# Performance work log

Measured on AMD Instinct MI355X. Metric: run time of the kernel, lower is better.

The kernel has to match this reference:

```python
import jax, jax.numpy as jnp
import numpy as np

B, D_IN, D_OUT, N_CTRL = 8192, 512, 512, 8

def setup_inputs() -> dict:
    key = jax.random.key(0)
    k1, k2, k3, k4 = jax.random.split(key, 4)
    inputs = jax.random.normal(k1, (B, D_IN), dtype=jnp.float32)
    # routing weights: positive soft blend coefficients, normalized per sample
    raw = jax.random.uniform(k2, (B, N_CTRL), dtype=jnp.float32)
    weights = raw / jnp.sum(raw, axis=-1, keepdims=True)
    w = jax.random.normal(k3, (N_CTRL, D_IN, D_OUT), dtype=jnp.float32) * 0.05
    b = jax.random.normal(k4, (N_CTRL, D_OUT), dtype=jnp.float32) * 0.05
    return {"inputs": inputs, "weights": weights, "w": w, "b": b}

def reference(inputs, weights, w, b):
    # Original math: w_p = einsum('ji,imk->jmk', weights, w)  [B, D_IN, D_OUT]
    #                out = squeeze(inputs[:, None, :] @ w_p) + weights @ b
    # Fused equivalent avoiding the [B, D_IN, D_OUT] intermediate:
    # run all n_control expert matmuls, then blend by routing weights.
    per_expert = jnp.einsum('bi,cio->cbo', inputs, w)       # [C, B, D_OUT]
    out = jnp.einsum('bc,cbo->bo', weights, per_expert)     # [B, D_OUT]
    out = out + weights @ b                                 # blended bias [B, D_OUT]
    return out
```

## Files before the change

### kernel.cpp

```cpp
#include <hip/hip_runtime.h>

#define B_   8192
#define DIN  512
#define DOUT 512
#define NC   8
#define NCD  (NC * DIN)
#define KSPL 4

typedef float  f32x4 __attribute__((ext_vector_type(4)));
typedef short  s16x8 __attribute__((ext_vector_type(8)));
typedef unsigned short u16x4 __attribute__((ext_vector_type(4)));
typedef unsigned int   u32x4 __attribute__((ext_vector_type(4)));

__device__ __forceinline__ unsigned short f2bf(float f) {
  unsigned u = __builtin_bit_cast(unsigned, f);
  u += 0x7fffu + ((u >> 16) & 1u);
  return (unsigned short)(u >> 16);
}
__device__ __forceinline__ float bf2f(unsigned short h) {
  unsigned u = ((unsigned)h) << 16;
  return __builtin_bit_cast(float, u);
}
__device__ __forceinline__ unsigned cvtpk(float lo, float hi) {
  unsigned r;
  asm("v_cvt_pk_bf16_f32 %0, %1, %2" : "=v"(r) : "v"(lo), "v"(hi));
  return r;
}

__global__ void pack_xw_k(const f32x4* __restrict__ x, u16x4* __restrict__ xb,
                          const float* __restrict__ w, unsigned short* __restrict__ WtF) {
  __shared__ float tile[64][65];
  const int tid = threadIdx.x;
  if (blockIdx.x < 4096) {
    int gid = blockIdx.x * 256 + tid;
    f32x4 v = x[gid];
    u16x4 o;
    o[0] = f2bf(v[0]); o[1] = f2bf(v[1]); o[2] = f2bf(v[2]); o[3] = f2bf(v[3]);
    xb[gid] = o;
    return;
  }
  const int idx = blockIdx.x - 4096;
  const int kb = idx & 63, nb = idx >> 6;
  const int e = kb >> 3, ktl = kb & 7;
#pragma unroll
  for (int it = 0; it < 16; ++it) {
    int u = it * 256 + tid;
    int r = u >> 6, cc = u & 63;
    tile[r][cc] = w[(size_t)(e * 512 + ktl * 64 + r) * DOUT + nb * 64 + cc];
  }
  __syncthreads();
#pragma unroll
  for (int it = 0; it < 2; ++it) {
    int c = it * 256 + tid;
    int n16l = c >> 7, kk = (c >> 6) & 1, l = c & 63;
    int l15 = l & 15, lhi = l >> 4;
    int col_in = n16l * 16 + l15;
    int k_in   = kk * 32 + lhi * 8;
    int n16    = nb * 4 + n16l;
    u16x4 o0, o1;
    o0[0] = f2bf(tile[k_in + 0][col_in]); o0[1] = f2bf(tile[k_in + 1][col_in]);
    o0[2] = f2bf(tile[k_in + 2][col_in]); o0[3] = f2bf(tile[k_in + 3][col_in]);
    o1[0] = f2bf(tile[k_in + 4][col_in]); o1[1] = f2bf(tile[k_in + 5][col_in]);
    o1[2] = f2bf(tile[k_in + 6][col_in]); o1[3] = f2bf(tile[k_in + 7][col_in]);
    size_t base = ((((size_t)e * 32 + n16) * 8 + ktl) * 2 + kk) * 512 + l * 8;
    *(u16x4*)(WtF + base)     = o0;
    *(u16x4*)(WtF + base + 4) = o1;
  }
}

__global__ __launch_bounds__(256) void gemm_k(
    const unsigned short* __restrict__ xb,
    const unsigned short* __restrict__ WtF,
    const float* __restrict__ wt,
    unsigned short* __restrict__ part) {
  extern __shared__ char smem[];
  const int tid  = threadIdx.x;
  const int lane = tid & 63, wid = tid >> 6;
  const int wm = wid >> 1, wn = wid & 1;
  const int l15 = lane & 15, lhi = lane >> 4;

  const int n0   = blockIdx.x;
  const int ks   = n0 & 3;
  const int bn   = (n0 >> 2) & 3;
  const int by   = n0 >> 4;
  const int brow = by * 128, bcol = bn * 128;

  const int srow = tid >> 3, schunk = tid & 7;
  const int swz  = schunk ^ (srow & 7);
  const unsigned short* gA = xb + (size_t)(brow + srow) * DIN + schunk * 8;
  const int adst_off = srow * 128 + swz * 16;

  const unsigned short* bn0 = WtF + (size_t)(ks * 2) * 262144
                                  + (size_t)(bn * 8 + wn * 4) * 8192 + lane * 8;
  const unsigned short* bn1 = bn0 + 8192;
  const unsigned short* bn2 = bn0 + 16384;
  const unsigned short* bn3 = bn0 + 24576;

  const float* wtp = wt + (size_t)(brow + srow) * NC + ks * 2;
  const float wtv0_0 = wtp[0],           wtv1_0 = wtp[1];
  const float wtv0_1 = wtp[32 * NC],     wtv1_1 = wtp[32 * NC + 1];
  const float wtv0_2 = wtp[64 * NC],     wtv1_2 = wtp[64 * NC + 1];
  const float wtv0_3 = wtp[96 * NC],     wtv1_3 = wtp[96 * NC + 1];

  f32x4 acc[4][4] = {};
  s16x8 areg0, areg1, areg2, areg3;
  s16x8 a[4], b0q[4], b1q[4];
  const int x7    = l15 & 7;
  const int pc0   = (lhi ^ x7) * 16;
  const int pc1   = ((4 + lhi) ^ x7) * 16;
  const int abase = (wm * 64 + l15) * 128;

#define LOAD_B(BQ, et, ktl, kk) {                                            \
    const size_t o_ = (size_t)(et) * 262144 + ((ktl) * 2 + (kk)) * 512;      \
    BQ[0] = *(const s16x8*)(bn0 + o_);                                       \
    BQ[1] = *(const s16x8*)(bn1 + o_);                                       \
    BQ[2] = *(const s16x8*)(bn2 + o_);                                       \
    BQ[3] = *(const s16x8*)(bn3 + o_); }
#define LOAD_AREGS(kt) {                                                     \
    const unsigned short* s_ = gA + ((kt) & 7) * 64;                         \
    areg0 = *(const s16x8*)(s_);                                             \
    areg1 = *(const s16x8*)(s_ + (size_t)32 * DIN);                          \
    areg2 = *(const s16x8*)(s_ + (size_t)64 * DIN);                          \
    areg3 = *(const s16x8*)(s_ + (size_t)96 * DIN); }
#define SCALE_STORE(AR, S, P, slotb) {                                       \
    u32x4 v_;                                                                \
    v_[0] = cvtpk(bf2f((unsigned short)AR[0]) * (S),                         \
                  bf2f((unsigned short)AR[1]) * (S));                        \
    v_[1] = cvtpk(bf2f((unsigned short)AR[2]) * (S),                         \
                  bf2f((unsigned short)AR[3]) * (S));                        \
    v_[2] = cvtpk(bf2f((unsigned short)AR[4]) * (S),                         \
                  bf2f((unsigned short)AR[5]) * (S));                        \
    v_[3] = cvtpk(bf2f((unsigned short)AR[6]) * (S),                         \
                  bf2f((unsigned short)AR[7]) * (S));                        \
    *(u32x4*)(smem + (slotb) + adst_off + (P) * 4096) = v_; }
#define SCALE_WRITE_ALL(e_, slotb) {                                         \
    SCALE_STORE(areg0, (e_) ? wtv1_0 : wtv0_0, 0, slotb);                    \
    SCALE_STORE(areg1, (e_) ? wtv1_1 : wtv0_1, 1, slotb);                    \
    SCALE_STORE(areg2, (e_) ? wtv1_2 : wtv0_2, 2, slotb);                    \
    SCALE_STORE(areg3, (e_) ? wtv1_3 : wtv0_3, 3, slotb); }
#define RD_A4(slotb, PC) {                                                   \
    const char* pa_ = smem + (slotb) + abase + (PC);                         \
    _Pragma("unroll") for (int m = 0; m < 4; ++m)                            \
      a[m] = *(const s16x8*)(pa_ + m * 2048); }
#define MFMA_HALF(BQ)                                                        \
    _Pragma("unroll") for (int m = 0; m < 4; ++m)                            \
      _Pragma("unroll") for (int n = 0; n < 4; ++n)                          \
        acc[m][n] = __builtin_amdgcn_mfma_f32_16x16x32_bf16(                 \
            a[m], BQ[n], acc[m][n], 0, 0, 0);

  LOAD_AREGS(0);
  SCALE_WRITE_ALL(0, 0);
  LOAD_AREGS(1);
  LOAD_B(b0q, 0, 0, 0);
  __syncthreads();

  for (int t = 0; t < 16; ++t) {
    const int ct = (t & 1) * 16384, ot = 16384 - ct;
    RD_A4(ct, pc0);
    LOAD_B(b1q, (t >> 3), (t & 7), 1);
    MFMA_HALF(b0q);
    if (t < 15) {
      SCALE_WRITE_ALL(((t + 1) >> 3), ot);
      if (t < 14) LOAD_AREGS(t + 2);
    }
    RD_A4(ct, pc1);
    MFMA_HALF(b1q);
    if (t < 15) LOAD_B(b0q, ((t + 1) >> 3), ((t + 1) & 7), 0);
    __syncthreads();
  }

  unsigned short* Cs = (unsigned short*)smem;
#pragma unroll
  for (int m = 0; m < 4; ++m)
#pragma unroll
    for (int n = 0; n < 4; ++n) {
      const int row = wm * 64 + m * 16 + lhi * 4;
      const int col = wn * 64 + n * 16 + l15;
      f32x4 v = acc[m][n];
#pragma unroll
      for (int j = 0; j < 4; ++j)
        Cs[(row + j) * 132 + col] = f2bf(v[j]);
    }
  __syncthreads();
  unsigned short* pc = part + (size_t)ks * (B_ * DOUT) + (size_t)brow * DOUT + bcol;
#pragma unroll
  for (int it = 0; it < 8; ++it) {
    const int u = it * 256 + tid;
    const int row = u >> 4, cu = (u & 15) * 8;
    f32x4 v = *(const f32x4*)(Cs + row * 132 + cu);
    *(f32x4*)(pc + (size_t)row * DOUT + cu) = v;
  }
#undef LOAD_B
#undef LOAD_AREGS
#undef SCALE_STORE
#undef SCALE_WRITE_ALL
#undef RD_A4
#undef MFMA_HALF
}

__global__ void reduce_k(const unsigned short* __restrict__ part,
                         const float* __restrict__ wt,
                         const float* __restrict__ bias,
                         float* __restrict__ out) {
  int gid = blockIdx.x * 256 + threadIdx.x;
  int b = gid >> 7;
  int o4 = (gid & 127) << 2;
  float w8[8];
  *(f32x4*)w8       = *(const f32x4*)(wt + (size_t)b * NC);
  *(f32x4*)(w8 + 4) = *(const f32x4*)(wt + (size_t)b * NC + 4);
  f32x4 acc = {0.f, 0.f, 0.f, 0.f};
  const size_t off = (size_t)b * DOUT + o4;
#pragma unroll
  for (int s = 0; s < KSPL; ++s) {
    u16x4 p = *(const u16x4*)(part + (size_t)s * (B_ * DOUT) + off);
#pragma unroll
    for (int i = 0; i < 4; ++i) acc[i] += bf2f(p[i]);
  }
#pragma unroll
  for (int cc = 0; cc < NC; ++cc) {
    f32x4 bi = *(const f32x4*)(bias + cc * DOUT + o4);
#pragma unroll
    for (int i = 0; i < 4; ++i) acc[i] += w8[cc] * bi[i];
  }
  *(f32x4*)(out + off) = acc;
}

__global__ void bias_only_k(const float* __restrict__ wt,
                            const float* __restrict__ bias,
                            float* __restrict__ out) {
  int gid = blockIdx.x * 256 + threadIdx.x;
  int b = gid >> 7;
  int o4 = (gid & 127) << 2;
  float w8[8];
  *(f32x4*)w8       = *(const f32x4*)(wt + (size_t)b * NC);
  *(f32x4*)(w8 + 4) = *(const f32x4*)(wt + (size_t)b * NC + 4);
  f32x4 acc = {0.f, 0.f, 0.f, 0.f};
#pragma unroll
  for (int cc = 0; cc < NC; ++cc) {
    f32x4 bi = *(const f32x4*)(bias + cc * DOUT + o4);
#pragma unroll
    for (int i = 0; i < 4; ++i) acc[i] += w8[cc] * bi[i];
  }
  *(f32x4*)(out + (size_t)b * DOUT + o4) = acc;
}

extern "C" void kernel_launch(void* const* d_in, const int* in_sizes, int n_in,
                              void* d_out, int out_size, void* d_ws, size_t ws_size,
                              hipStream_t stream) {
  const float *x = nullptr, *wtc = nullptr, *w = nullptr, *bias = nullptr;
  for (int i = 0; i < n_in; ++i) {
    switch (in_sizes[i]) {
      case B_ * DIN:        x    = (const float*)d_in[i]; break;
      case B_ * NC:         wtc  = (const float*)d_in[i]; break;
      case NC * DIN * DOUT: w    = (const float*)d_in[i]; break;
      case NC * DOUT:       bias = (const float*)d_in[i]; break;
    }
  }
  float* out = (float*)d_out;

  const size_t XB_ELEMS   = (size_t)B_ * DIN;
  const size_t WT_ELEMS   = (size_t)NC * DIN * DOUT;
  const size_t PART_ELEMS = (size_t)KSPL * B_ * DOUT;
  const size_t need = (XB_ELEMS + WT_ELEMS + PART_ELEMS) * sizeof(unsigned short);

  if (ws_size < need) {
    bias_only_k<<<(B_ * DOUT / 4) / 256, 256, 0, stream>>>(wtc, bias, out);
    return;
  }

  unsigned short* xb   = (unsigned short*)d_ws;
  unsigned short* WtF  = xb + XB_ELEMS;
  unsigned short* part = WtF + WT_ELEMS;

  const int GEMM_LDS = 128 * 132 * 2;
  (void)hipFuncSetAttribute((const void*)gemm_k,
                            hipFuncAttributeMaxDynamicSharedMemorySize, GEMM_LDS);

  pack_xw_k<<<4096 + 512, 256, 0, stream>>>((const f32x4*)x, (u16x4*)xb, w, WtF);
  gemm_k<<<1024, 256, GEMM_LDS, stream>>>(xb, WtF, wtc, part);
  reduce_k<<<(B_ * DOUT / 4) / 256, 256, 0, stream>>>(part, wtc, bias, out);
}
```

Before: 75.04 us.

## Drop split-K and fuse bias blend into GEMM epilogue, removing reduce kernel

```diff
diff --git a/kernel.cpp b/kernel.cpp
--- a/kernel.cpp
+++ b/kernel.cpp
@@ -4,8 +4,6 @@
 #define DIN  512
 #define DOUT 512
 #define NC   8
-#define NCD  (NC * DIN)
-#define KSPL 4
 
 typedef float  f32x4 __attribute__((ext_vector_type(4)));
 typedef short  s16x8 __attribute__((ext_vector_type(8)));
@@ -72,56 +70,48 @@
     const unsigned short* __restrict__ xb,
     const unsigned short* __restrict__ WtF,
     const float* __restrict__ wt,
-    unsigned short* __restrict__ part) {
+    const float* __restrict__ bias,
+    float* __restrict__ out) {
   extern __shared__ char smem[];
   const int tid  = threadIdx.x;
-  const int lane = tid & 63, wid = tid >> 6;
-  const int wm = wid >> 1, wn = wid & 1;
+  const int lane = tid & 63, wn = tid >> 6;
   const int l15 = lane & 15, lhi = lane >> 4;
 
   const int n0   = blockIdx.x;
-  const int ks   = n0 & 3;
-  const int bn   = (n0 >> 2) & 3;
-  const int by   = n0 >> 4;
-  const int brow = by * 128, bcol = bn * 128;
+  const int by   = n0 >> 1, bn = n0 & 1;
+  const int brow = by * 64, bcol = bn * 256;
 
   const int srow = tid >> 3, schunk = tid & 7;
   const int swz  = schunk ^ (srow & 7);
   const unsigned short* gA = xb + (size_t)(brow + srow) * DIN + schunk * 8;
   const int adst_off = srow * 128 + swz * 16;
 
-  const unsigned short* bn0 = WtF + (size_t)(ks * 2) * 262144
-                                  + (size_t)(bn * 8 + wn * 4) * 8192 + lane * 8;
-  const unsigned short* bn1 = bn0 + 8192;
-  const unsigned short* bn2 = bn0 + 16384;
-  const unsigned short* bn3 = bn0 + 24576;
-
-  const float* wtp = wt + (size_t)(brow + srow) * NC + ks * 2;
-  const float wtv0_0 = wtp[0],           wtv1_0 = wtp[1];
-  const float wtv0_1 = wtp[32 * NC],     wtv1_1 = wtp[32 * NC + 1];
-  const float wtv0_2 = wtp[64 * NC],     wtv1_2 = wtp[64 * NC + 1];
-  const float wtv0_3 = wtp[96 * NC],     wtv1_3 = wtp[96 * NC + 1];
+  const unsigned short* bq0 = WtF + (size_t)(bn * 16 + wn * 4) * 8192 + lane * 8;
+  const unsigned short* bq1 = bq0 + 8192;
+  const unsigned short* bq2 = bq0 + 16384;
+  const unsigned short* bq3 = bq0 + 24576;
+
+  const float* gwA = wt + (size_t)(brow + srow) * NC;
+  const float* gwB = gwA + 32 * NC;
 
   f32x4 acc[4][4] = {};
-  s16x8 areg0, areg1, areg2, areg3;
+  s16x8 areg0, areg1;
   s16x8 a[4], b0q[4], b1q[4];
   const int x7    = l15 & 7;
   const int pc0   = (lhi ^ x7) * 16;
   const int pc1   = ((4 + lhi) ^ x7) * 16;
-  const int abase = (wm * 64 + l15) * 128;
+  const int abase = l15 * 128;
 
 #define LOAD_B(BQ, et, ktl, kk) {                                            \
     const size_t o_ = (size_t)(et) * 262144 + ((ktl) * 2 + (kk)) * 512;      \
-    BQ[0] = *(const s16x8*)(bn0 + o_);                                       \
-    BQ[1] = *(const s16x8*)(bn1 + o_);                                       \
-    BQ[2] = *(const s16x8*)(bn2 + o_);                                       \
-    BQ[3] = *(const s16x8*)(bn3 + o_); }
+    BQ[0] = *(const s16x8*)(bq0 + o_);                                       \
+    BQ[1] = *(const s16x8*)(bq1 + o_);                                       \
+    BQ[2] = *(const s16x8*)(bq2 + o_);                                       \
+    BQ[3] = *(const s16x8*)(bq3 + o_); }
 #define LOAD_AREGS(kt) {                                                     \
     const unsigned short* s_ = gA + ((kt) & 7) * 64;                         \
     areg0 = *(const s16x8*)(s_);                                             \
-    areg1 = *(const s16x8*)(s_ + (size_t)32 * DIN);                          \
-    areg2 = *(const s16x8*)(s_ + (size_t)64 * DIN);                          \
-    areg3 = *(const s16x8*)(s_ + (size_t)96 * DIN); }
+    areg1 = *(const s16x8*)(s_ + (size_t)32 * DIN); }
 #define SCALE_STORE(AR, S, P, slotb) {                                       \
     u32x4 v_;                                                                \
     v_[0] = cvtpk(bf2f((unsigned short)AR[0]) * (S),                         \
@@ -133,11 +123,9 @@
     v_[3] = cvtpk(bf2f((unsigned short)AR[6]) * (S),                         \
                   bf2f((unsigned short)AR[7]) * (S));                        \
     *(u32x4*)(smem + (slotb) + adst_off + (P) * 4096) = v_; }
-#define SCALE_WRITE_ALL(e_, slotb) {                                         \
-    SCALE_STORE(areg0, (e_) ? wtv1_0 : wtv0_0, 0, slotb);                    \
-    SCALE_STORE(areg1, (e_) ? wtv1_1 : wtv0_1, 1, slotb);                    \
-    SCALE_STORE(areg2, (e_) ? wtv1_2 : wtv0_2, 2, slotb);                    \
-    SCALE_STORE(areg3, (e_) ? wtv1_3 : wtv0_3, 3, slotb); }
+#define SCALE_WRITE2(SA, SB, slotb) {                                        \
+    SCALE_STORE(areg0, SA, 0, slotb);                                        \
+    SCALE_STORE(areg1, SB, 1, slotb); }
 #define RD_A4(slotb, PC) {                                                   \
     const char* pa_ = smem + (slotb) + abase + (PC);                         \
     _Pragma("unroll") for (int m = 0; m < 4; ++m)                            \
@@ -148,81 +136,70 @@
         acc[m][n] = __builtin_amdgcn_mfma_f32_16x16x32_bf16(                 \
             a[m], BQ[n], acc[m][n], 0, 0, 0);
 
+  float wAc = gwA[0], wBc = gwB[0], wAn = 0.f, wBn = 0.f;
   LOAD_AREGS(0);
-  SCALE_WRITE_ALL(0, 0);
+  SCALE_WRITE2(wAc, wBc, 0);
   LOAD_AREGS(1);
   LOAD_B(b0q, 0, 0, 0);
   __syncthreads();
 
-  for (int t = 0; t < 16; ++t) {
-    const int ct = (t & 1) * 16384, ot = 16384 - ct;
+#pragma unroll 2
+  for (int t = 0; t < 64; ++t) {
+    const int ct = (t & 1) * 8192, ot = 8192 - ct;
     RD_A4(ct, pc0);
-    LOAD_B(b1q, (t >> 3), (t & 7), 1);
+    LOAD_B(b1q, t >> 3, t & 7, 1);
     MFMA_HALF(b0q);
-    if (t < 15) {
-      SCALE_WRITE_ALL(((t + 1) >> 3), ot);
-      if (t < 14) LOAD_AREGS(t + 2);
-    }
+    if ((t & 7) == 0 && t < 56) {
+      wAn = gwA[(t + 8) >> 3]; wBn = gwB[(t + 8) >> 3];
+    }
+    if (t < 63) {
+      const float sA = ((t & 7) == 7) ? wAn : wAc;
+      const float sB = ((t & 7) == 7) ? wBn : wBc;
+      SCALE_WRITE2(sA, sB, ot);
+      if (t < 62) LOAD_AREGS(t + 2);
+    }
+    if ((t & 7) == 7) { wAc = wAn; wBc = wBn; }
     RD_A4(ct, pc1);
     MFMA_HALF(b1q);
-    if (t < 15) LOAD_B(b0q, ((t + 1) >> 3), ((t + 1) & 7), 0);
+    if (t < 63) LOAD_B(b0q, (t + 1) >> 3, (t + 1) & 7, 0);
     __syncthreads();
   }
 
-  unsigned short* Cs = (unsigned short*)smem;
+  float* Cs = (float*)smem;
 #pragma unroll
   for (int m = 0; m < 4; ++m)
 #pragma unroll
     for (int n = 0; n < 4; ++n) {
-      const int row = wm * 64 + m * 16 + lhi * 4;
+      const int row = m * 16 + lhi * 4;
       const int col = wn * 64 + n * 16 + l15;
       f32x4 v = acc[m][n];
 #pragma unroll
       for (int j = 0; j < 4; ++j)
-        Cs[(row + j) * 132 + col] = f2bf(v[j]);
+        Cs[(row + j) * 260 + col] = v[j];
     }
   __syncthreads();
-  unsigned short* pc = part + (size_t)ks * (B_ * DOUT) + (size_t)brow * DOUT + bcol;
-#pragma unroll
-  for (int it = 0; it < 8; ++it) {
-    const int u = it * 256 + tid;
-    const int row = u >> 4, cu = (u & 15) * 8;
-    f32x4 v = *(const f32x4*)(Cs + row * 132 + cu);
-    *(f32x4*)(pc + (size_t)row * DOUT + cu) = v;
+#pragma unroll
+  for (int it = 0; it < 16; ++it) {
+    const int u   = it * 256 + tid;
+    const int row = u >> 6, ch = u & 63;
+    const int grow = brow + row, gcol = bcol + ch * 4;
+    f32x4 v = *(const f32x4*)(Cs + row * 260 + ch * 4);
+    const float* w8p = wt + (size_t)grow * NC;
+#pragma unroll
+    for (int c = 0; c < NC; ++c) {
+      const float wc = w8p[c];
+      f32x4 bv = *(const f32x4*)(bias + c * DOUT + gcol);
+#pragma unroll
+      for (int i = 0; i < 4; ++i) v[i] += wc * bv[i];
+    }
+    *(f32x4*)(out + (size_t)grow * DOUT + gcol) = v;
   }
 #undef LOAD_B
 #undef LOAD_AREGS
 #undef SCALE_STORE
-#undef SCALE_WRITE_ALL
+#undef SCALE_WRITE2
 #undef RD_A4
 #undef MFMA_HALF
-}
-
-__global__ void reduce_k(const unsigned short* __restrict__ part,
-                         const float* __restrict__ wt,
-                         const float* __restrict__ bias,
-                         float* __restrict__ out) {
-  int gid = blockIdx.x * 256 + threadIdx.x;
-  int b = gid >> 7;
-  int o4 = (gid & 127) << 2;
-  float w8[8];
-  *(f32x4*)w8       = *(const f32x4*)(wt + (size_t)b * NC);
-  *(f32x4*)(w8 + 4) = *(const f32x4*)(wt + (size_t)b * NC + 4);
-  f32x4 acc = {0.f, 0.f, 0.f, 0.f};
-  const size_t off = (size_t)b * DOUT + o4;
-#pragma unroll
-  for (int s = 0; s < KSPL; ++s) {
-    u16x4 p = *(const u16x4*)(part + (size_t)s * (B_ * DOUT) + off);
-#pragma unroll
-    for (int i = 0; i < 4; ++i) acc[i] += bf2f(p[i]);
-  }
-#pragma unroll
-  for (int cc = 0; cc < NC; ++cc) {
-    f32x4 bi = *(const f32x4*)(bias + cc * DOUT + o4);
-#pragma unroll
-    for (int i = 0; i < 4; ++i) acc[i] += w8[cc] * bi[i];
-  }
-  *(f32x4*)(out + off) = acc;
 }
 
 __global__ void bias_only_k(const float* __restrict__ wt,
@@ -258,25 +235,22 @@
   }
   float* out = (float*)d_out;
 
-  const size_t XB_ELEMS   = (size_t)B_ * DIN;
-  const size_t WT_ELEMS   = (size_t)NC * DIN * DOUT;
-  const size_t PART_ELEMS = (size_t)KSPL * B_ * DOUT;
-  const size_t need = (XB_ELEMS + WT_ELEMS + PART_ELEMS) * sizeof(unsigned short);
+  const size_t XB_ELEMS = (size_t)B_ * DIN;
+  const size_t WT_ELEMS = (size_t)NC * DIN * DOUT;
+  const size_t need = (XB_ELEMS + WT_ELEMS) * sizeof(unsigned short);
 
   if (ws_size < need) {
     bias_only_k<<<(B_ * DOUT / 4) / 256, 256, 0, stream>>>(wtc, bias, out);
     return;
   }
 
-  unsigned short* xb   = (unsigned short*)d_ws;
-  unsigned short* WtF  = xb + XB_ELEMS;
-  unsigned short* part = WtF + WT_ELEMS;
-
-  const int GEMM_LDS = 128 * 132 * 2;
+  unsigned short* xb  = (unsigned short*)d_ws;
+  unsigned short* WtF = xb + XB_ELEMS;
+
+  const int GEMM_LDS = 64 * 260 * 4;
   (void)hipFuncSetAttribute((const void*)gemm_k,
                             hipFuncAttributeMaxDynamicSharedMemorySize, GEMM_LDS);
 
   pack_xw_k<<<4096 + 512, 256, 0, stream>>>((const f32x4*)x, (u16x4*)xb, w, WtF);
-  gemm_k<<<1024, 256, GEMM_LDS, stream>>>(xb, WtF, wtc, part);
-  reduce_k<<<(B_ * DOUT / 4) / 256, 256, 0, stream>>>(part, wtc, bias, out);
-}
+  gemm_k<<<256, 256, GEMM_LDS, stream>>>(xb, WtF, wtc, bias, out);
+}
```

After: 100.0 us. 33.3% more time.

## Widen GEMM block tile to 128x256 with 8 waves and single B buffer

Applied to the files above, without the earlier changes.

```diff
diff --git a/kernel.cpp b/kernel.cpp
--- a/kernel.cpp
+++ b/kernel.cpp
@@ -4,7 +4,6 @@
 #define DIN  512
 #define DOUT 512
 #define NC   8
-#define NCD  (NC * DIN)
 #define KSPL 4
 
 typedef float  f32x4 __attribute__((ext_vector_type(4)));
@@ -68,7 +67,7 @@
   }
 }
 
-__global__ __launch_bounds__(256) void gemm_k(
+__global__ __launch_bounds__(512, 2) void gemm_k(
     const unsigned short* __restrict__ xb,
     const unsigned short* __restrict__ WtF,
     const float* __restrict__ wt,
@@ -76,35 +75,32 @@
   extern __shared__ char smem[];
   const int tid  = threadIdx.x;
   const int lane = tid & 63, wid = tid >> 6;
-  const int wm = wid >> 1, wn = wid & 1;
+  const int wm = wid >> 2, wn = wid & 3;
   const int l15 = lane & 15, lhi = lane >> 4;
 
   const int n0   = blockIdx.x;
   const int ks   = n0 & 3;
-  const int bn   = (n0 >> 2) & 3;
-  const int by   = n0 >> 4;
-  const int brow = by * 128, bcol = bn * 128;
-
-  const int srow = tid >> 3, schunk = tid & 7;
-  const int swz  = schunk ^ (srow & 7);
-  const unsigned short* gA = xb + (size_t)(brow + srow) * DIN + schunk * 8;
-  const int adst_off = srow * 128 + swz * 16;
-
-  const unsigned short* bn0 = WtF + (size_t)(ks * 2) * 262144
-                                  + (size_t)(bn * 8 + wn * 4) * 8192 + lane * 8;
-  const unsigned short* bn1 = bn0 + 8192;
-  const unsigned short* bn2 = bn0 + 16384;
-  const unsigned short* bn3 = bn0 + 24576;
-
-  const float* wtp = wt + (size_t)(brow + srow) * NC + ks * 2;
-  const float wtv0_0 = wtp[0],           wtv1_0 = wtp[1];
-  const float wtv0_1 = wtp[32 * NC],     wtv1_1 = wtp[32 * NC + 1];
-  const float wtv0_2 = wtp[64 * NC],     wtv1_2 = wtp[64 * NC + 1];
-  const float wtv0_3 = wtp[96 * NC],     wtv1_3 = wtp[96 * NC + 1];
+  const int bn   = (n0 >> 2) & 1;
+  const int by   = n0 >> 3;
+  const int brow = by * 128, bcol = bn * 256;
+
+  const int srow = tid >> 2, sc = tid & 3;
+  const int swz  = sc ^ (srow & 7);
+  const unsigned short* gA = xb + (size_t)(brow + srow) * DIN + sc * 8;
+  const int adst0 = srow * 128 + swz * 16;
+
+  const unsigned short* bq0 = WtF + (size_t)(ks * 2) * 262144
+                                  + (size_t)(bn * 16 + wn * 4) * 8192 + lane * 8;
+  const unsigned short* bq1 = bq0 + 8192;
+  const unsigned short* bq2 = bq0 + 16384;
+  const unsigned short* bq3 = bq0 + 24576;
+
+  const float wtv0 = wt[(size_t)(brow + srow) * NC + ks * 2];
+  const float wtv1 = wt[(size_t)(brow + srow) * NC + ks * 2 + 1];
 
   f32x4 acc[4][4] = {};
-  s16x8 areg0, areg1, areg2, areg3;
-  s16x8 a[4], b0q[4], b1q[4];
+  s16x8 areg0, areg1;
+  s16x8 a[4], b[4];
   const int x7    = l15 & 7;
   const int pc0   = (lhi ^ x7) * 16;
   const int pc1   = ((4 + lhi) ^ x7) * 16;
@@ -112,17 +108,15 @@
 
 #define LOAD_B(BQ, et, ktl, kk) {                                            \
     const size_t o_ = (size_t)(et) * 262144 + ((ktl) * 2 + (kk)) * 512;      \
-    BQ[0] = *(const s16x8*)(bn0 + o_);                                       \
-    BQ[1] = *(const s16x8*)(bn1 + o_);                                       \
-    BQ[2] = *(const s16x8*)(bn2 + o_);                                       \
-    BQ[3] = *(const s16x8*)(bn3 + o_); }
+    BQ[0] = *(const s16x8*)(bq0 + o_);                                       \
+    BQ[1] = *(const s16x8*)(bq1 + o_);                                       \
+    BQ[2] = *(const s16x8*)(bq2 + o_);                                       \
+    BQ[3] = *(const s16x8*)(bq3 + o_); }
 #define LOAD_AREGS(kt) {                                                     \
     const unsigned short* s_ = gA + ((kt) & 7) * 64;                         \
     areg0 = *(const s16x8*)(s_);                                             \
-    areg1 = *(const s16x8*)(s_ + (size_t)32 * DIN);                          \
-    areg2 = *(const s16x8*)(s_ + (size_t)64 * DIN);                          \
-    areg3 = *(const s16x8*)(s_ + (size_t)96 * DIN); }
-#define SCALE_STORE(AR, S, P, slotb) {                                       \
+    areg1 = *(const s16x8*)(s_ + 32); }
+#define SCALE_STORE(AR, S, DST) {                                            \
     u32x4 v_;                                                                \
     v_[0] = cvtpk(bf2f((unsigned short)AR[0]) * (S),                         \
                   bf2f((unsigned short)AR[1]) * (S));                        \
@@ -132,40 +126,39 @@
                   bf2f((unsigned short)AR[5]) * (S));                        \
     v_[3] = cvtpk(bf2f((unsigned short)AR[6]) * (S),                         \
                   bf2f((unsigned short)AR[7]) * (S));                        \
-    *(u32x4*)(smem + (slotb) + adst_off + (P) * 4096) = v_; }
-#define SCALE_WRITE_ALL(e_, slotb) {                                         \
-    SCALE_STORE(areg0, (e_) ? wtv1_0 : wtv0_0, 0, slotb);                    \
-    SCALE_STORE(areg1, (e_) ? wtv1_1 : wtv0_1, 1, slotb);                    \
-    SCALE_STORE(areg2, (e_) ? wtv1_2 : wtv0_2, 2, slotb);                    \
-    SCALE_STORE(areg3, (e_) ? wtv1_3 : wtv0_3, 3, slotb); }
+    *(u32x4*)(smem + (DST)) = v_; }
+#define SCALE_WRITE(e_, slotb) {                                             \
+    const float s_ = (e_) ? wtv1 : wtv0;                                     \
+    SCALE_STORE(areg0, s_, (slotb) + adst0);                                 \
+    SCALE_STORE(areg1, s_, (slotb) + (adst0 ^ 64)); }
 #define RD_A4(slotb, PC) {                                                   \
     const char* pa_ = smem + (slotb) + abase + (PC);                         \
     _Pragma("unroll") for (int m = 0; m < 4; ++m)                            \
       a[m] = *(const s16x8*)(pa_ + m * 2048); }
-#define MFMA_HALF(BQ)                                                        \
+#define MFMA_HALF()                                                          \
     _Pragma("unroll") for (int m = 0; m < 4; ++m)                            \
       _Pragma("unroll") for (int n = 0; n < 4; ++n)                          \
         acc[m][n] = __builtin_amdgcn_mfma_f32_16x16x32_bf16(                 \
-            a[m], BQ[n], acc[m][n], 0, 0, 0);
+            a[m], b[n], acc[m][n], 0, 0, 0);
 
   LOAD_AREGS(0);
-  SCALE_WRITE_ALL(0, 0);
+  SCALE_WRITE(0, 0);
   LOAD_AREGS(1);
-  LOAD_B(b0q, 0, 0, 0);
   __syncthreads();
 
   for (int t = 0; t < 16; ++t) {
     const int ct = (t & 1) * 16384, ot = 16384 - ct;
+    const int et = t >> 3, ktl = t & 7;
+    LOAD_B(b, et, ktl, 0);
     RD_A4(ct, pc0);
-    LOAD_B(b1q, (t >> 3), (t & 7), 1);
-    MFMA_HALF(b0q);
+    MFMA_HALF();
+    LOAD_B(b, et, ktl, 1);
+    RD_A4(ct, pc1);
     if (t < 15) {
-      SCALE_WRITE_ALL(((t + 1) >> 3), ot);
+      SCALE_WRITE(((t + 1) >> 3), ot);
       if (t < 14) LOAD_AREGS(t + 2);
     }
-    RD_A4(ct, pc1);
-    MFMA_HALF(b1q);
-    if (t < 15) LOAD_B(b0q, ((t + 1) >> 3), ((t + 1) & 7), 0);
+    MFMA_HALF();
     __syncthreads();
   }
 
@@ -179,21 +172,21 @@
       f32x4 v = acc[m][n];
 #pragma unroll
       for (int j = 0; j < 4; ++j)
-        Cs[(row + j) * 132 + col] = f2bf(v[j]);
+        Cs[(row + j) * 264 + col] = f2bf(v[j]);
     }
   __syncthreads();
   unsigned short* pc = part + (size_t)ks * (B_ * DOUT) + (size_t)brow * DOUT + bcol;
 #pragma unroll
   for (int it = 0; it < 8; ++it) {
-    const int u = it * 256 + tid;
-    const int row = u >> 4, cu = (u & 15) * 8;
-    f32x4 v = *(const f32x4*)(Cs + row * 132 + cu);
+    const int u = it * 512 + tid;
+    const int row = u >> 5, cu = (u & 31) * 8;
+    f32x4 v = *(const f32x4*)(Cs + row * 264 + cu);
     *(f32x4*)(pc + (size_t)row * DOUT + cu) = v;
   }
 #undef LOAD_B
 #undef LOAD_AREGS
 #undef SCALE_STORE
-#undef SCALE_WRITE_ALL
+#undef SCALE_WRITE
 #undef RD_A4
 #undef MFMA_HALF
 }
@@ -272,11 +265,11 @@
   unsigned short* WtF  = xb + XB_ELEMS;
   unsigned short* part = WtF + WT_ELEMS;
 
-  const int GEMM_LDS = 128 * 132 * 2;
+  const int GEMM_LDS = 128 * 264 * 2;
   (void)hipFuncSetAttribute((const void*)gemm_k,
                             hipFuncAttributeMaxDynamicSharedMemorySize, GEMM_LDS);
 
   pack_xw_k<<<4096 + 512, 256, 0, stream>>>((const f32x4*)x, (u16x4*)xb, w, WtF);
-  gemm_k<<<1024, 256, GEMM_LDS, stream>>>(xb, WtF, wtc, part);
+  gemm_k<<<512, 512, GEMM_LDS, stream>>>(xb, WtF, wtc, part);
   reduce_k<<<(B_ * DOUT / 4) / 256, 256, 0, stream>>>(part, wtc, bias, out);
 }
```

After: 78.66 us. 4.8% more time.
